# Optimization experiments

Hardware: AMD Instinct MI355X
Metric: run time of the kernel (lower is better)

Reference implementation:

```python
import jax, jax.numpy as jnp
import numpy as np

CTX_LEN = 256
N_EMBED = 256
HEAD_SIZE = 64
DROPOUT_RATE = 0.25
BATCH = 512
SEQ = 256  # T <= CTX_LEN


def setup_inputs() -> dict:
    key = jax.random.key(0)
    k1, k2, k3, k4, k5 = jax.random.split(key, 5)
    x = jax.random.normal(k1, (BATCH, SEQ, N_EMBED), dtype=jnp.float32)
    # Linear(bias=False) weights, stored as [in, out] so y = x @ W
    Wq = jax.random.normal(k2, (N_EMBED, HEAD_SIZE), dtype=jnp.float32) * (N_EMBED ** -0.5)
    Wk = jax.random.normal(k3, (N_EMBED, HEAD_SIZE), dtype=jnp.float32) * (N_EMBED ** -0.5)
    Wv = jax.random.normal(k4, (N_EMBED, HEAD_SIZE), dtype=jnp.float32) * (N_EMBED ** -0.5)
    # uniform noise for deterministic dropout: keep where mask >= p
    dropout_mask = jax.random.uniform(k5, (BATCH, SEQ, SEQ), dtype=jnp.float32)
    return {"x": x, "Wq": Wq, "Wk": Wk, "Wv": Wv, "dropout_mask": dropout_mask}


def reference(x, Wq, Wk, Wv, dropout_mask):
    B, T, C = x.shape
    q = x @ Wq                                   # [B,T,H]
    k = x @ Wk                                   # [B,T,H]
    v = x @ Wv                                   # [B,T,H]
    scale = k.shape[-1] ** -0.5
    wei = jnp.einsum('btd,bsd->bts', q, k) * scale  # [B,T,T]
    causal = jnp.tril(jnp.ones((T, T), dtype=bool))
    wei = jnp.where(causal, wei, -jnp.inf)
    wei = jax.nn.softmax(wei, axis=-1)
    # dropout (train mode): zero with prob p, scale survivors by 1/(1-p)
    keep = dropout_mask >= DROPOUT_RATE
    wei = jnp.where(keep, wei, 0.0) / (1.0 - DROPOUT_RATE)
    out = jnp.einsum('bts,bsd->btd', wei, v)     # [B,T,H]
    return out
```

## Files before the change

kernel.cpp:

```cpp
#include <hip/hip_runtime.h>
#include <hip/hip_bf16.h>

typedef __attribute__((ext_vector_type(8))) short short8;
typedef __attribute__((ext_vector_type(4))) float f32x4;
typedef __attribute__((ext_vector_type(4))) unsigned short ushort4v;
typedef unsigned short u16;
typedef unsigned int u32;

#define MFMA32(a, b, c) __builtin_amdgcn_mfma_f32_16x16x32_bf16((a), (b), (c), 0, 0, 0)

__device__ __forceinline__ u16 f2bf(float f) {
    __hip_bfloat16 h = __float2bfloat16(f);
    return *reinterpret_cast<u16*>(&h);
}
__device__ __forceinline__ u32 pack2(float a, float b) {
    return ((u32)f2bf(b) << 16) | (u32)f2bf(a);
}

__device__ __forceinline__ void tile_step(int c2, int t_my, int lr, int lg,
                                          const int* adr,
                                          const short8* qf,
                                          const u16 (*lk)[72],
                                          const u16 (*lvT)[264],
                                          const float* mb,
                                          float& ls, f32x4* O)
{
    f32x4 md0 = *(const f32x4*)&mb[(size_t)t_my * 256 + 32 * c2 + 4 * lg];
    f32x4 md1 = *(const f32x4*)&mb[(size_t)t_my * 256 + 32 * c2 + 16 + 4 * lg];

    f32x4 S0, S1;
    {
        const u16* kr = &lk[16 * (2 * c2) + lr][0];
        short8 kf0 = *(const short8*)&kr[8 * lg];
        short8 kf1 = *(const short8*)&kr[32 + 8 * lg];
        f32x4 a = (f32x4){0.f, 0.f, 0.f, 0.f};
        a = MFMA32(kf0, qf[0], a);
        a = MFMA32(kf1, qf[1], a);
        S0 = a;
    }
    {
        const u16* kr = &lk[16 * (2 * c2 + 1) + lr][0];
        short8 kf0 = *(const short8*)&kr[8 * lg];
        short8 kf1 = *(const short8*)&kr[32 + 8 * lg];
        f32x4 a = (f32x4){0.f, 0.f, 0.f, 0.f};
        a = MFMA32(kf0, qf[0], a);
        a = MFMA32(kf1, qf[1], a);
        S1 = a;
    }

    #pragma unroll
    for (int j = 0; j < 4; ++j) {
        const int sg0 = 32 * c2 + 4 * lg + j;
        const int sg1 = sg0 + 16;
        float p0 = exp2f(S0[j] * 0.180336879f);
        float p1 = exp2f(S1[j] * 0.180336879f);
        p0 = (sg0 <= t_my) ? p0 : 0.f;
        p1 = (sg1 <= t_my) ? p1 : 0.f;
        ls += p0 + p1;
        S0[j] = (md0[j] >= 0.25f) ? p0 : 0.f;
        S1[j] = (md1[j] >= 0.25f) ? p1 : 0.f;
    }

    u32 pk0[2], pk1[2];
    pk0[0] = pack2(S0[0], S0[1]); pk0[1] = pack2(S0[2], S0[3]);
    pk1[0] = pack2(S1[0], S1[1]); pk1[1] = pack2(S1[2], S1[3]);
    union { u32 u[4]; short8 s; } pf;
    #pragma unroll
    for (int e = 0; e < 4; ++e) {
        u32 ca = (u32)__builtin_amdgcn_ds_bpermute(adr[e], (int)pk0[e & 1]);
        u32 cb = (u32)__builtin_amdgcn_ds_bpermute(adr[e], (int)pk1[e & 1]);
        pf.u[e] = (lg >> 1) ? cb : ca;
    }

    #pragma unroll
    for (int ht = 0; ht < 4; ++ht) {
        short8 vf = *(const short8*)&lvT[16 * ht + lr][32 * c2 + 8 * lg];
        O[ht] = MFMA32(vf, pf.s, O[ht]);
    }
}

__device__ __forceinline__ void attn_dual(int tA, int tB, int lr, int lg,
                                          const int* adr,
                                          const short8* qfA, const short8* qfB,
                                          const u16 (*lk)[72],
                                          const u16 (*lvT)[264],
                                          const float* mb, float* ob)
{
    const int nchA = (tA + 2) >> 1;
    const int nchB = (tB + 2) >> 1;
    const int tmA  = 16 * tA + lr;
    const int tmB  = 16 * tB + lr;

    float lsA = 0.f, lsB = 0.f;
    f32x4 OA[4], OB[4];
    #pragma unroll
    for (int ht = 0; ht < 4; ++ht) {
        OA[ht] = (f32x4){0.f, 0.f, 0.f, 0.f};
        OB[ht] = (f32x4){0.f, 0.f, 0.f, 0.f};
    }

    int c2 = 0;
    for (; c2 < nchA; ++c2) {
        tile_step(c2, tmB, lr, lg, adr, qfB, lk, lvT, mb, lsB, OB);
        tile_step(c2, tmA, lr, lg, adr, qfA, lk, lvT, mb, lsA, OA);
    }
    for (; c2 < nchB; ++c2)
        tile_step(c2, tmB, lr, lg, adr, qfB, lk, lvT, mb, lsB, OB);

    lsA += __shfl_xor(lsA, 16, 64);
    lsA += __shfl_xor(lsA, 32, 64);
    lsB += __shfl_xor(lsB, 16, 64);
    lsB += __shfl_xor(lsB, 32, 64);

    const float rfA = 1.33333333333f / lsA;
    const float rfB = 1.33333333333f / lsB;
    #pragma unroll
    for (int ht = 0; ht < 4; ++ht) {
        f32x4 oa  = OA[ht] * rfA;
        f32x4 obv = OB[ht] * rfB;
        *(f32x4*)&ob[(size_t)tmA * 64 + 16 * ht + 4 * lg] = oa;
        *(f32x4*)&ob[(size_t)tmB * 64 + 16 * ht + 4 * lg] = obv;
    }
}

#define STAGE_W(Wm) do {                                                     \
    _Pragma("unroll")                                                        \
    for (int i_ = 0; i_ < 4; ++i_) {                                         \
        const int c0_ = 8 * (w + 8 * i_);                                    \
        short8 t_;                                                           \
        _Pragma("unroll")                                                    \
        for (int j_ = 0; j_ < 8; ++j_)                                       \
            t_[j_] = (short)f2bf((Wm)[(size_t)(c0_ + j_) * 64 + l]);         \
        *(short8*)&wt[l][c0_] = t_;                                          \
    } } while (0)

__global__ __launch_bounds__(512, 2)
void attn_head_fused(const float* __restrict__ x,
                     const float* __restrict__ Wq,
                     const float* __restrict__ Wk,
                     const float* __restrict__ Wv,
                     const float* __restrict__ dmask,
                     float* __restrict__ out)
{
    __shared__ __align__(16) u16 lk[256][72];
    __shared__ __align__(16) u16 lvT[64][264];
    __shared__ __align__(16) u16 wt[64][264];

    const int b   = blockIdx.x;
    const int tid = threadIdx.x;
    const int w   = tid >> 6;
    const int l   = tid & 63;
    const int lr  = l & 15;
    const int lg  = l >> 4;

    const int TbA = 16 * w;
    const int TbB = 16 * (15 - w);

    const float* xb = x + (size_t)b * 65536;

    int adr[4];
    #pragma unroll
    for (int e = 0; e < 4; ++e) {
        const int lgp = ((8 * lg + 2 * e) & 15) >> 2;
        adr[e] = 4 * (lr + 16 * lgp);
    }

    short8 af[2][8];
    #pragma unroll
    for (int ti = 0; ti < 2; ++ti) {
        const float* xr = xb + (size_t)((ti ? TbB : TbA) + lr) * 256 + lg * 8;
        #pragma unroll
        for (int ks = 0; ks < 8; ++ks) {
            f32x4 a0 = *(const f32x4*)(xr + ks * 32);
            f32x4 a1 = *(const f32x4*)(xr + ks * 32 + 4);
            short8 f;
            f[0] = (short)f2bf(a0[0]); f[1] = (short)f2bf(a0[1]);
            f[2] = (short)f2bf(a0[2]); f[3] = (short)f2bf(a0[3]);
            f[4] = (short)f2bf(a1[0]); f[5] = (short)f2bf(a1[1]);
            f[6] = (short)f2bf(a1[2]); f[7] = (short)f2bf(a1[3]);
            af[ti][ks] = f;
        }
    }

    f32x4 acc[2][4];

    STAGE_W(Wk);
    __syncthreads();
    #pragma unroll
    for (int ti = 0; ti < 2; ++ti)
        #pragma unroll
        for (int nj = 0; nj < 4; ++nj) acc[ti][nj] = (f32x4){0.f,0.f,0.f,0.f};
    #pragma unroll
    for (int ks = 0; ks < 8; ++ks)
        #pragma unroll
        for (int nj = 0; nj < 4; ++nj) {
            short8 bf = *(const short8*)&wt[16 * nj + lr][ks * 32 + lg * 8];
            acc[0][nj] = MFMA32(af[0][ks], bf, acc[0][nj]);
            acc[1][nj] = MFMA32(af[1][ks], bf, acc[1][nj]);
        }
    #pragma unroll
    for (int nj = 0; nj < 4; ++nj) {
        const int n = 16 * nj + lr;
        #pragma unroll
        for (int j = 0; j < 4; ++j) {
            lk[TbA + 4 * lg + j][n] = f2bf(acc[0][nj][j]);
            lk[TbB + 4 * lg + j][n] = f2bf(acc[1][nj][j]);
        }
    }
    __syncthreads();

    STAGE_W(Wv);
    __syncthreads();
    #pragma unroll
    for (int ti = 0; ti < 2; ++ti)
        #pragma unroll
        for (int nj = 0; nj < 4; ++nj) acc[ti][nj] = (f32x4){0.f,0.f,0.f,0.f};
    #pragma unroll
    for (int ks = 0; ks < 8; ++ks)
        #pragma unroll
        for (int nj = 0; nj < 4; ++nj) {
            short8 bf = *(const short8*)&wt[16 * nj + lr][ks * 32 + lg * 8];
            acc[0][nj] = MFMA32(af[0][ks], bf, acc[0][nj]);
            acc[1][nj] = MFMA32(af[1][ks], bf, acc[1][nj]);
        }
    #pragma unroll
    for (int ti = 0; ti < 2; ++ti) {
        const int s0 = (ti ? TbB : TbA) + 4 * lg;
        #pragma unroll
        for (int nj = 0; nj < 4; ++nj) {
            ushort4v pk;
            pk[0] = f2bf(acc[ti][nj][0]);
            pk[1] = f2bf(acc[ti][nj][1]);
            pk[2] = f2bf(acc[ti][nj][2]);
            pk[3] = f2bf(acc[ti][nj][3]);
            *(ushort4v*)&lvT[16 * nj + lr][s0] = pk;
        }
    }
    __syncthreads();

    STAGE_W(Wq);
    __syncthreads();
    #pragma unroll
    for (int ti = 0; ti < 2; ++ti)
        #pragma unroll
        for (int nj = 0; nj < 4; ++nj) acc[ti][nj] = (f32x4){0.f,0.f,0.f,0.f};
    #pragma unroll
    for (int ks = 0; ks < 8; ++ks)
        #pragma unroll
        for (int nj = 0; nj < 4; ++nj) {
            short8 bf = *(const short8*)&wt[16 * nj + lr][ks * 32 + lg * 8];
            acc[0][nj] = MFMA32(bf, af[0][ks], acc[0][nj]);
            acc[1][nj] = MFMA32(bf, af[1][ks], acc[1][nj]);
        }
    short8 qf[2][2];
    #pragma unroll
    for (int ti = 0; ti < 2; ++ti) {
        u32 qk[4][2];
        #pragma unroll
        for (int nj = 0; nj < 4; ++nj) {
            qk[nj][0] = pack2(acc[ti][nj][0], acc[ti][nj][1]);
            qk[nj][1] = pack2(acc[ti][nj][2], acc[ti][nj][3]);
        }
        union { u32 u[4]; short8 s; } q0, q1;
        #pragma unroll
        for (int e = 0; e < 4; ++e) {
            u32 a0 = (u32)__builtin_amdgcn_ds_bpermute(adr[e], (int)qk[0][e & 1]);
            u32 a1 = (u32)__builtin_amdgcn_ds_bpermute(adr[e], (int)qk[1][e & 1]);
            q0.u[e] = (lg >> 1) ? a1 : a0;
            u32 b0 = (u32)__builtin_amdgcn_ds_bpermute(adr[e], (int)qk[2][e & 1]);
            u32 b1 = (u32)__builtin_amdgcn_ds_bpermute(adr[e], (int)qk[3][e & 1]);
            q1.u[e] = (lg >> 1) ? b1 : b0;
        }
        qf[ti][0] = q0.s; qf[ti][1] = q1.s;
    }

    const float* mb = dmask + (size_t)b * 65536;
    float* ob = out + (size_t)b * 16384;

    attn_dual(w, 15 - w, lr, lg, adr, qf[0], qf[1], lk, lvT, mb, ob);
}

extern "C" void kernel_launch(void* const* d_in, const int* in_sizes, int n_in,
                              void* d_out, int out_size, void* d_ws, size_t ws_size,
                              hipStream_t stream) {
    const float* x  = (const float*)d_in[0];
    const float* Wq = (const float*)d_in[1];
    const float* Wk = (const float*)d_in[2];
    const float* Wv = (const float*)d_in[3];
    const float* dm = (const float*)d_in[4];
    float* outp     = (float*)d_out;
    attn_head_fused<<<dim3(512), dim3(512), 0, stream>>>(x, Wq, Wk, Wv, dm, outp);
}
```

Baseline: 54.37 us.

## Process two batches per block and prefetch next batch's x during attention

Each block now handles two batch elements in sequence, with 256 blocks launched instead of 512. The second batch's x rows are loaded into registers while the first batch's attention runs, to hide global load latency. Launch bounds drop to one block per CU to make room for the extra 32 prefetch vector registers. The cost is lower occupancy and only 256 blocks on a 256-CU device, so each CU runs a single block and has less latency hiding from other blocks.

```diff
diff --git a/kernel.cpp b/kernel.cpp
--- a/kernel.cpp
+++ b/kernel.cpp
@@ -134,7 +134,118 @@
         *(short8*)&wt[l][c0_] = t_;                                          \
     } } while (0)
 
-__global__ __launch_bounds__(512, 2)
+#define ISSUE_X(dst, xb_, Tbase) do {                                        \
+    const float* xr_ = (xb_) + (size_t)((Tbase) + lr) * 256 + lg * 8;        \
+    _Pragma("unroll")                                                        \
+    for (int ks_ = 0; ks_ < 8; ++ks_) {                                      \
+        dst[2 * ks_]     = *(const f32x4*)(xr_ + ks_ * 32);                  \
+        dst[2 * ks_ + 1] = *(const f32x4*)(xr_ + ks_ * 32 + 4);              \
+    } } while (0)
+
+#define CVT_X(af_, src) do {                                                 \
+    _Pragma("unroll")                                                        \
+    for (int ks_ = 0; ks_ < 8; ++ks_) {                                      \
+        f32x4 a0_ = src[2 * ks_], a1_ = src[2 * ks_ + 1];                    \
+        short8 f_;                                                           \
+        f_[0] = (short)f2bf(a0_[0]); f_[1] = (short)f2bf(a0_[1]);            \
+        f_[2] = (short)f2bf(a0_[2]); f_[3] = (short)f2bf(a0_[3]);            \
+        f_[4] = (short)f2bf(a1_[0]); f_[5] = (short)f2bf(a1_[1]);            \
+        f_[6] = (short)f2bf(a1_[2]); f_[7] = (short)f2bf(a1_[3]);            \
+        (af_)[ks_] = f_;                                                     \
+    } } while (0)
+
+#define DO_PROJ(qf_) do {                                                    \
+    f32x4 acc[2][4];                                                         \
+    STAGE_W(Wk);                                                             \
+    __syncthreads();                                                         \
+    _Pragma("unroll")                                                        \
+    for (int ti = 0; ti < 2; ++ti)                                           \
+        _Pragma("unroll")                                                    \
+        for (int nj = 0; nj < 4; ++nj) acc[ti][nj] = (f32x4){0.f,0.f,0.f,0.f}; \
+    _Pragma("unroll")                                                        \
+    for (int ks = 0; ks < 8; ++ks)                                           \
+        _Pragma("unroll")                                                    \
+        for (int nj = 0; nj < 4; ++nj) {                                     \
+            short8 bf = *(const short8*)&wt[16 * nj + lr][ks * 32 + lg * 8]; \
+            acc[0][nj] = MFMA32(af[0][ks], bf, acc[0][nj]);                  \
+            acc[1][nj] = MFMA32(af[1][ks], bf, acc[1][nj]);                  \
+        }                                                                    \
+    _Pragma("unroll")                                                        \
+    for (int nj = 0; nj < 4; ++nj) {                                         \
+        const int n = 16 * nj + lr;                                          \
+        _Pragma("unroll")                                                    \
+        for (int j = 0; j < 4; ++j) {                                        \
+            lk[TbA + 4 * lg + j][n] = f2bf(acc[0][nj][j]);                   \
+            lk[TbB + 4 * lg + j][n] = f2bf(acc[1][nj][j]);                   \
+        }                                                                    \
+    }                                                                        \
+    __syncthreads();                                                         \
+    STAGE_W(Wv);                                                             \
+    __syncthreads();                                                         \
+    _Pragma("unroll")                                                        \
+    for (int ti = 0; ti < 2; ++ti)                                           \
+        _Pragma("unroll")                                                    \
+        for (int nj = 0; nj < 4; ++nj) acc[ti][nj] = (f32x4){0.f,0.f,0.f,0.f}; \
+    _Pragma("unroll")                                                        \
+    for (int ks = 0; ks < 8; ++ks)                                           \
+        _Pragma("unroll")                                                    \
+        for (int nj = 0; nj < 4; ++nj) {                                     \
+            short8 bf = *(const short8*)&wt[16 * nj + lr][ks * 32 + lg * 8]; \
+            acc[0][nj] = MFMA32(af[0][ks], bf, acc[0][nj]);                  \
+            acc[1][nj] = MFMA32(af[1][ks], bf, acc[1][nj]);                  \
+        }                                                                    \
+    _Pragma("unroll")                                                        \
+    for (int ti = 0; ti < 2; ++ti) {                                         \
+        const int s0 = (ti ? TbB : TbA) + 4 * lg;                            \
+        _Pragma("unroll")                                                    \
+        for (int nj = 0; nj < 4; ++nj) {                                     \
+            ushort4v pk;                                                     \
+            pk[0] = f2bf(acc[ti][nj][0]);                                    \
+            pk[1] = f2bf(acc[ti][nj][1]);                                    \
+            pk[2] = f2bf(acc[ti][nj][2]);                                    \
+            pk[3] = f2bf(acc[ti][nj][3]);                                    \
+            *(ushort4v*)&lvT[16 * nj + lr][s0] = pk;                         \
+        }                                                                    \
+    }                                                                        \
+    __syncthreads();                                                         \
+    STAGE_W(Wq);                                                             \
+    __syncthreads();                                                         \
+    _Pragma("unroll")                                                        \
+    for (int ti = 0; ti < 2; ++ti)                                           \
+        _Pragma("unroll")                                                    \
+        for (int nj = 0; nj < 4; ++nj) acc[ti][nj] = (f32x4){0.f,0.f,0.f,0.f}; \
+    _Pragma("unroll")                                                        \
+    for (int ks = 0; ks < 8; ++ks)                                           \
+        _Pragma("unroll")                                                    \
+        for (int nj = 0; nj < 4; ++nj) {                                     \
+            short8 bf = *(const short8*)&wt[16 * nj + lr][ks * 32 + lg * 8]; \
+            acc[0][nj] = MFMA32(bf, af[0][ks], acc[0][nj]);                  \
+            acc[1][nj] = MFMA32(bf, af[1][ks], acc[1][nj]);                  \
+        }                                                                    \
+    _Pragma("unroll")                                                        \
+    for (int ti = 0; ti < 2; ++ti) {                                         \
+        u32 qk[4][2];                                                        \
+        _Pragma("unroll")                                                    \
+        for (int nj = 0; nj < 4; ++nj) {                                     \
+            qk[nj][0] = pack2(acc[ti][nj][0], acc[ti][nj][1]);               \
+            qk[nj][1] = pack2(acc[ti][nj][2], acc[ti][nj][3]);               \
+        }                                                                    \
+        union { u32 u[4]; short8 s; } q0_, q1_;                              \
+        _Pragma("unroll")                                                    \
+        for (int e = 0; e < 4; ++e) {                                        \
+            u32 a0 = (u32)__builtin_amdgcn_ds_bpermute(adr[e], (int)qk[0][e & 1]); \
+            u32 a1 = (u32)__builtin_amdgcn_ds_bpermute(adr[e], (int)qk[1][e & 1]); \
+            q0_.u[e] = (lg >> 1) ? a1 : a0;                                  \
+            u32 b0 = (u32)__builtin_amdgcn_ds_bpermute(adr[e], (int)qk[2][e & 1]); \
+            u32 b1 = (u32)__builtin_amdgcn_ds_bpermute(adr[e], (int)qk[3][e & 1]); \
+            q1_.u[e] = (lg >> 1) ? b1 : b0;                                  \
+        }                                                                    \
+        qf_[ti][0] = q0_.s; qf_[ti][1] = q1_.s;                              \
+    }                                                                        \
+    __syncthreads();                       \
+    } while (0)
+
+__global__ __launch_bounds__(512, 1)
 void attn_head_fused(const float* __restrict__ x,
                      const float* __restrict__ Wq,
                      const float* __restrict__ Wk,
@@ -146,7 +257,8 @@
     __shared__ __align__(16) u16 lvT[64][264];
     __shared__ __align__(16) u16 wt[64][264];
 
-    const int b   = blockIdx.x;
+    const int b0  = blockIdx.x;
+    const int b1  = blockIdx.x + 256;
     const int tid = threadIdx.x;
     const int w   = tid >> 6;
     const int l   = tid & 63;
@@ -156,7 +268,8 @@
     const int TbA = 16 * w;
     const int TbB = 16 * (15 - w);
 
-    const float* xb = x + (size_t)b * 65536;
+    const float* xb0 = x + (size_t)b0 * 65536;
+    const float* xb1 = x + (size_t)b1 * 65536;
 
     int adr[4];
     #pragma unroll
@@ -165,119 +278,32 @@
         adr[e] = 4 * (lr + 16 * lgp);
     }
 
+    f32x4 xpA[16], xpB[16];
     short8 af[2][8];
-    #pragma unroll
-    for (int ti = 0; ti < 2; ++ti) {
-        const float* xr = xb + (size_t)((ti ? TbB : TbA) + lr) * 256 + lg * 8;
-        #pragma unroll
-        for (int ks = 0; ks < 8; ++ks) {
-            f32x4 a0 = *(const f32x4*)(xr + ks * 32);
-            f32x4 a1 = *(const f32x4*)(xr + ks * 32 + 4);
-            short8 f;
-            f[0] = (short)f2bf(a0[0]); f[1] = (short)f2bf(a0[1]);
-            f[2] = (short)f2bf(a0[2]); f[3] = (short)f2bf(a0[3]);
-            f[4] = (short)f2bf(a1[0]); f[5] = (short)f2bf(a1[1]);
-            f[6] = (short)f2bf(a1[2]); f[7] = (short)f2bf(a1[3]);
-            af[ti][ks] = f;
-        }
-    }
-
-    f32x4 acc[2][4];
-
-    STAGE_W(Wk);
+    short8 qf[2][2];
+
+    ISSUE_X(xpA, xb0, TbA);
+    ISSUE_X(xpB, xb0, TbB);
+    CVT_X(af[0], xpA);
+    CVT_X(af[1], xpB);
+
+    DO_PROJ(qf);
+
+    ISSUE_X(xpA, xb1, TbA);
+    ISSUE_X(xpB, xb1, TbB);
+
+    attn_dual(w, 15 - w, lr, lg, adr, qf[0], qf[1], lk, lvT,
+              dmask + (size_t)b0 * 65536, out + (size_t)b0 * 16384);
+
     __syncthreads();
-    #pragma unroll
-    for (int ti = 0; ti < 2; ++ti)
-        #pragma unroll
-        for (int nj = 0; nj < 4; ++nj) acc[ti][nj] = (f32x4){0.f,0.f,0.f,0.f};
-    #pragma unroll
-    for (int ks = 0; ks < 8; ++ks)
-        #pragma unroll
-        for (int nj = 0; nj < 4; ++nj) {
-            short8 bf = *(const short8*)&wt[16 * nj + lr][ks * 32 + lg * 8];
-            acc[0][nj] = MFMA32(af[0][ks], bf, acc[0][nj]);
-            acc[1][nj] = MFMA32(af[1][ks], bf, acc[1][nj]);
-        }
-    #pragma unroll
-    for (int nj = 0; nj < 4; ++nj) {
-        const int n = 16 * nj + lr;
-        #pragma unroll
-        for (int j = 0; j < 4; ++j) {
-            lk[TbA + 4 * lg + j][n] = f2bf(acc[0][nj][j]);
-            lk[TbB + 4 * lg + j][n] = f2bf(acc[1][nj][j]);
-        }
-    }
-    __syncthreads();
-
-    STAGE_W(Wv);
-    __syncthreads();
-    #pragma unroll
-    for (int ti = 0; ti < 2; ++ti)
-        #pragma unroll
-        for (int nj = 0; nj < 4; ++nj) acc[ti][nj] = (f32x4){0.f,0.f,0.f,0.f};
-    #pragma unroll
-    for (int ks = 0; ks < 8; ++ks)
-        #pragma unroll
-        for (int nj = 0; nj < 4; ++nj) {
-            short8 bf = *(const short8*)&wt[16 * nj + lr][ks * 32 + lg * 8];
-            acc[0][nj] = MFMA32(af[0][ks], bf, acc[0][nj]);
-            acc[1][nj] = MFMA32(af[1][ks], bf, acc[1][nj]);
-        }
-    #pragma unroll
-    for (int ti = 0; ti < 2; ++ti) {
-        const int s0 = (ti ? TbB : TbA) + 4 * lg;
-        #pragma unroll
-        for (int nj = 0; nj < 4; ++nj) {
-            ushort4v pk;
-            pk[0] = f2bf(acc[ti][nj][0]);
-            pk[1] = f2bf(acc[ti][nj][1]);
-            pk[2] = f2bf(acc[ti][nj][2]);
-            pk[3] = f2bf(acc[ti][nj][3]);
-            *(ushort4v*)&lvT[16 * nj + lr][s0] = pk;
-        }
-    }
-    __syncthreads();
-
-    STAGE_W(Wq);
-    __syncthreads();
-    #pragma unroll
-    for (int ti = 0; ti < 2; ++ti)
-        #pragma unroll
-        for (int nj = 0; nj < 4; ++nj) acc[ti][nj] = (f32x4){0.f,0.f,0.f,0.f};
-    #pragma unroll
-    for (int ks = 0; ks < 8; ++ks)
-        #pragma unroll
-        for (int nj = 0; nj < 4; ++nj) {
-            short8 bf = *(const short8*)&wt[16 * nj + lr][ks * 32 + lg * 8];
-            acc[0][nj] = MFMA32(bf, af[0][ks], acc[0][nj]);
-            acc[1][nj] = MFMA32(bf, af[1][ks], acc[1][nj]);
-        }
-    short8 qf[2][2];
-    #pragma unroll
-    for (int ti = 0; ti < 2; ++ti) {
-        u32 qk[4][2];
-        #pragma unroll
-        for (int nj = 0; nj < 4; ++nj) {
-            qk[nj][0] = pack2(acc[ti][nj][0], acc[ti][nj][1]);
-            qk[nj][1] = pack2(acc[ti][nj][2], acc[ti][nj][3]);
-        }
-        union { u32 u[4]; short8 s; } q0, q1;
-        #pragma unroll
-        for (int e = 0; e < 4; ++e) {
-            u32 a0 = (u32)__builtin_amdgcn_ds_bpermute(adr[e], (int)qk[0][e & 1]);
-            u32 a1 = (u32)__builtin_amdgcn_ds_bpermute(adr[e], (int)qk[1][e & 1]);
-            q0.u[e] = (lg >> 1) ? a1 : a0;
-            u32 b0 = (u32)__builtin_amdgcn_ds_bpermute(adr[e], (int)qk[2][e & 1]);
-            u32 b1 = (u32)__builtin_amdgcn_ds_bpermute(adr[e], (int)qk[3][e & 1]);
-            q1.u[e] = (lg >> 1) ? b1 : b0;
-        }
-        qf[ti][0] = q0.s; qf[ti][1] = q1.s;
-    }
-
-    const float* mb = dmask + (size_t)b * 65536;
-    float* ob = out + (size_t)b * 16384;
-
-    attn_dual(w, 15 - w, lr, lg, adr, qf[0], qf[1], lk, lvT, mb, ob);
+
+    CVT_X(af[0], xpA);
+    CVT_X(af[1], xpB);
+
+    DO_PROJ(qf);
+
+    attn_dual(w, 15 - w, lr, lg, adr, qf[0], qf[1], lk, lvT,
+              dmask + (size_t)b1 * 65536, out + (size_t)b1 * 16384);
 }
 
 extern "C" void kernel_launch(void* const* d_in, const int* in_sizes, int n_in,
@@ -289,5 +315,5 @@
     const float* Wv = (const float*)d_in[3];
     const float* dm = (const float*)d_in[4];
     float* outp     = (float*)d_out;
-    attn_head_fused<<<dim3(512), dim3(512), 0, stream>>>(x, Wq, Wk, Wv, dm, outp);
-}
+    attn_head_fused<<<dim3(256), dim3(512), 0, stream>>>(x, Wq, Wk, Wv, dm, outp);
+}
```

Measured after the change: 100.9 us. 85.6% more time.
